# Performance work log

Hardware: AMD Instinct MI355X
Metric: run time of the kernel (lower is better)

Reference implementation:

```python
import jax, jax.numpy as jnp
import numpy as np

B, T, N, F_IN = 4, 8, 2048, 16
HID, HEADS, OUT_CH, OUT_FEAT = 128, 4, 64, 14
E = 32768


def _ln(x, g, b, eps=1e-5):
    mu = x.mean(-1, keepdims=True)
    var = ((x - mu) ** 2).mean(-1, keepdims=True)
    return (x - mu) / jnp.sqrt(var + eps) * g + b


def _attn_steps(x, wq, bq, wk, bk, wv, bv, wo, bo):
    # x: [B, S, M, F]; single-head causal attention over axis 1 (the 'steps' axis)
    q = x @ wq + bq
    k = x @ wk + bk
    v = x @ wv + bv
    scale = 1.0 / np.sqrt(q.shape[-1]).astype(np.float32)
    scores = jnp.einsum('bsmh,btmh->bmst', q, k) * scale  # [B,M,S,S]
    S = scores.shape[-1]
    scores = jnp.where(jnp.tril(jnp.ones((S, S), bool)), scores, -jnp.inf)
    a = jax.nn.softmax(scores, axis=-1)
    ctx = jnp.einsum('bmst,btmh->bsmh', a, v)
    return ctx @ wo + bo


def _attn_nodes(x, wq, bq, wk, bk, wv, bv, wo, bo):
    # single-head attention over axis 2 (the 'nodes' axis)
    q = x @ wq + bq
    k = x @ wk + bk
    v = x @ wv + bv
    scale = 1.0 / np.sqrt(q.shape[-1]).astype(np.float32)
    scores = jnp.einsum('bsnh,bsmh->bsnm', q, k) * scale
    a = jax.nn.softmax(scores, axis=-1)
    ctx = jnp.einsum('bsnm,bsmh->bsnh', a, v)
    return ctx @ wo + bo


def _gat(h, src, dst, n, W, a_src, a_dst, bias, heads, out_ch, concat):
    # PyG GATConv: gather src/dst features per edge, segment softmax over
    # incoming edges of each target node, weighted scatter-aggregate.
    hw = (h @ W).reshape(n, heads, out_ch)
    al_s = (hw * a_src).sum(-1)  # [n, heads]
    al_d = (hw * a_dst).sum(-1)
    loop = jnp.arange(n, dtype=src.dtype)
    src_f = jnp.concatenate([src, loop])
    dst_f = jnp.concatenate([dst, loop])
    alpha = jax.nn.leaky_relu(al_s[src_f] + al_d[dst_f], 0.2)
    # PyG removes pre-existing self-loops then adds canonical ones: mask them out.
    drop = jnp.concatenate([src == dst, jnp.zeros((n,), bool)])[:, None]
    amax = jax.lax.stop_gradient(
        jax.ops.segment_max(jnp.where(drop, -jnp.inf, alpha), dst_f, num_segments=n))
    ex = jnp.where(drop, 0.0, jnp.exp(alpha - amax[dst_f]))
    denom = jax.ops.segment_sum(ex, dst_f, num_segments=n)
    w = ex / denom[dst_f]  # [E_total, heads]
    out = jax.ops.segment_sum(hw[src_f] * w[:, :, None], dst_f, num_segments=n)
    if concat:
        return out.reshape(n, heads * out_ch) + bias
    return out.mean(1) + bias


def _forward(x, edge_index, ln1_g, ln1_b, t_wq, t_bq, t_wk, t_bk, t_wv, t_bv, t_wo, t_bo,
             skip_w, skip_b, ln2_g, ln2_b, s_wq, s_bq, s_wk, s_bk, s_wv, s_bv, s_wo, s_bo,
             ln3_g, ln3_b, mlp_w1, mlp_b1, mlp_w2, mlp_b2,
             gat1_w, gat1_asrc, gat1_adst, gat1_b, gat2_w, gat2_asrc, gat2_adst, gat2_b,
             ffn_w, ffn_b):
    Bx, Tx, Nx, _ = x.shape
    h = jnp.transpose(x, (0, 2, 1, 3))  # [B, N(steps), T(nodes), F]
    h = (h @ skip_w + skip_b) + _attn_steps(_ln(h, ln1_g, ln1_b),
                                            t_wq, t_bq, t_wk, t_bk, t_wv, t_bv, t_wo, t_bo)
    h = h + _attn_nodes(_ln(h, ln2_g, ln2_b), s_wq, s_bq, s_wk, s_bk, s_wv, s_bv, s_wo, s_bo)
    z = _ln(h, ln3_g, ln3_b)
    h = h + (jax.nn.relu(z @ mlp_w1 + mlp_b1) @ mlp_w2 + mlp_b2)
    h = h[:, :, -1, :].reshape(Bx * Nx, HID)  # last 'nodes'(=T) slot, flatten graphs
    src, dst = edge_index[0], edge_index[1]
    off = jnp.repeat(jnp.arange(Bx, dtype=src.dtype) * Nx, src.shape[0])
    src_b = jnp.tile(src, Bx) + off
    dst_b = jnp.tile(dst, Bx) + off
    nt = Bx * Nx
    g1 = jax.nn.elu(_gat(h, src_b, dst_b, nt, gat1_w, gat1_asrc, gat1_adst, gat1_b,
                         HEADS, HID // HEADS, True))
    g2 = _gat(g1, src_b, dst_b, nt, gat2_w, gat2_asrc, gat2_adst, gat2_b, 1, OUT_CH, False)
    out = g2.reshape(Bx, Nx, OUT_CH) @ ffn_w + ffn_b
    return jnp.transpose(out, (0, 2, 1))  # [B, output_features, N]


def setup_inputs():
    key = jax.random.key(0)
    ki = iter(list(jax.random.split(key, 40)))
    def rn(shape, s=0.05):
        return jax.random.normal(next(ki), shape, jnp.float32) * s
    d = {}
    d['x'] = jax.random.normal(next(ki), (B, T, N, F_IN), jnp.float32)
    d['edge_index'] = jax.random.randint(next(ki), (2, E), 0, N, jnp.int32)
    d['ln1_g'] = jnp.ones((F_IN,), jnp.float32); d['ln1_b'] = jnp.zeros((F_IN,), jnp.float32)
    d['t_wq'] = rn((F_IN, HID)); d['t_bq'] = jnp.zeros((HID,), jnp.float32)
    d['t_wk'] = rn((F_IN, HID)); d['t_bk'] = jnp.zeros((HID,), jnp.float32)
    d['t_wv'] = rn((F_IN, HID)); d['t_bv'] = jnp.zeros((HID,), jnp.float32)
    d['t_wo'] = rn((HID, HID)); d['t_bo'] = jnp.zeros((HID,), jnp.float32)
    d['skip_w'] = rn((F_IN, HID)); d['skip_b'] = jnp.zeros((HID,), jnp.float32)
    d['ln2_g'] = jnp.ones((HID,), jnp.float32); d['ln2_b'] = jnp.zeros((HID,), jnp.float32)
    d['s_wq'] = rn((HID, HID)); d['s_bq'] = jnp.zeros((HID,), jnp.float32)
    d['s_wk'] = rn((HID, HID)); d['s_bk'] = jnp.zeros((HID,), jnp.float32)
    d['s_wv'] = rn((HID, HID)); d['s_bv'] = jnp.zeros((HID,), jnp.float32)
    d['s_wo'] = rn((HID, HID)); d['s_bo'] = jnp.zeros((HID,), jnp.float32)
    d['ln3_g'] = jnp.ones((HID,), jnp.float32); d['ln3_b'] = jnp.zeros((HID,), jnp.float32)
    d['mlp_w1'] = rn((HID, 2 * HID)); d['mlp_b1'] = jnp.zeros((2 * HID,), jnp.float32)
    d['mlp_w2'] = rn((2 * HID, HID)); d['mlp_b2'] = jnp.zeros((HID,), jnp.float32)
    d['gat1_w'] = rn((HID, HID))
    d['gat1_asrc'] = rn((HEADS, HID // HEADS)); d['gat1_adst'] = rn((HEADS, HID // HEADS))
    d['gat1_b'] = jnp.zeros((HID,), jnp.float32)
    d['gat2_w'] = rn((HID, OUT_CH))
    d['gat2_asrc'] = rn((1, OUT_CH)); d['gat2_adst'] = rn((1, OUT_CH))
    d['gat2_b'] = jnp.zeros((OUT_CH,), jnp.float32)
    d['ffn_w'] = rn((OUT_CH, OUT_FEAT)); d['ffn_b'] = jnp.zeros((OUT_FEAT,), jnp.float32)
    return d


def reference(x, edge_index, ln1_g, ln1_b, t_wq, t_bq, t_wk, t_bk, t_wv, t_bv, t_wo, t_bo,
              skip_w, skip_b, ln2_g, ln2_b, s_wq, s_bq, s_wk, s_bk, s_wv, s_bv, s_wo, s_bo,
              ln3_g, ln3_b, mlp_w1, mlp_b1, mlp_w2, mlp_b2,
              gat1_w, gat1_asrc, gat1_adst, gat1_b, gat2_w, gat2_asrc, gat2_adst, gat2_b,
              ffn_w, ffn_b):
    return _forward(x, edge_index, ln1_g, ln1_b, t_wq, t_bq, t_wk, t_bk, t_wv, t_bv, t_wo, t_bo,
                    skip_w, skip_b, ln2_g, ln2_b, s_wq, s_bq, s_wk, s_bk, s_wv, s_bv, s_wo, s_bo,
                    ln3_g, ln3_b, mlp_w1, mlp_b1, mlp_w2, mlp_b2,
                    gat1_w, gat1_asrc, gat1_adst, gat1_b, gat2_w, gat2_asrc, gat2_adst, gat2_b,
                    ffn_w, ffn_b)
```

## Files before the change

kernel.cpp:

```cpp
#include <hip/hip_runtime.h>
#include <hip/hip_bf16.h>
#include <stdint.h>


#define BB     4
#define TT     8
#define NN     2048
#define FIN    16
#define HID    128
#define BM     (BB*TT)
#define PROWS  (BM*NN)
#define NHEADS 4
#define OUTCH  64
#define OUTF   14
#define NEDGE  32768
#define NEDGEB (NEDGE*BB)
#define NNODE  (BB*NN)
#define NETOT  (NEDGEB + NNODE)

#define TQ     64
#define NTILE  (NN/TQ)

typedef __hip_bfloat16 bf16;
typedef __attribute__((ext_vector_type(8))) short bf16x8;
typedef __attribute__((ext_vector_type(4))) float f32x4;

__device__ __forceinline__ float b2f(bf16 v){ return __bfloat162float(v); }
__device__ __forceinline__ bf16  f2b(float f){ return __float2bfloat16(f); }
__device__ __forceinline__ unsigned short bfbits(float f){
    union { bf16 h; unsigned short u; } cv; cv.h = f2b(f); return cv.u;
}

__global__ __launch_bounds__(256)
void k_kv(const float* __restrict__ x,
          const float* __restrict__ g1, const float* __restrict__ bb1,
          const float* __restrict__ wk, const float* __restrict__ bk,
          const float* __restrict__ wv, const float* __restrict__ bv,
          int in_off, bf16* __restrict__ K, bf16* __restrict__ Vt)
{
    const int r0 = blockIdx.x * 32;
    const int t  = threadIdx.x;

    __shared__ float wk_s[FIN][HID];
    __shared__ float wv_s[FIN][HID];
    __shared__ float xr_s[32][FIN+1];
    __shared__ float ln_s[32][FIN+1];

    #pragma unroll
    for (int it = 0; it < 2; ++it){
        const int u = t + it*256;
        ((float4*)wk_s)[u] = ((const float4*)wk)[u];
        ((float4*)wv_s)[u] = ((const float4*)wv)[u];
    }
    #pragma unroll
    for (int it = 0; it < 2; ++it){
        const int u = t + it*256;
        xr_s[u >> 4][u & 15] = x[(size_t)(r0 + in_off)*FIN + u];
    }
    __syncthreads();

    if (t < 32){
        float mu = 0.f;
        #pragma unroll
        for (int f = 0; f < FIN; ++f) mu += xr_s[t][f];
        mu *= (1.f/FIN);
        float var = 0.f;
        #pragma unroll
        for (int f = 0; f < FIN; ++f){ float d = xr_s[t][f]-mu; var += d*d; }
        var *= (1.f/FIN);
        const float inv = rsqrtf(var + 1e-5f);
        #pragma unroll
        for (int f = 0; f < FIN; ++f)
            ln_s[t][f] = (xr_s[t][f]-mu)*inv*g1[f] + bb1[f];
    }
    __syncthreads();

    {
        const int hk = (t & 63)*2;
        const float2 bkv = *(const float2*)&bk[hk];
        #pragma unroll
        for (int pass = 0; pass < 8; ++pass){
            const int key = pass*4 + (t >> 6);
            float a0 = bkv.x, a1 = bkv.y;
            #pragma unroll
            for (int f = 0; f < FIN; ++f){
                const float l = ln_s[key][f];
                const float2 wkv = ((const float2*)&wk_s[f][0])[t & 63];
                a0 += l*wkv.x; a1 += l*wkv.y;
            }
            const unsigned int pk =
                (unsigned int)bfbits(a0) | ((unsigned int)bfbits(a1) << 16);
            *(unsigned int*)(void*)&K[((size_t)(r0 + key))*HID + hk] = pk;
        }
    }

    {
        const int slice = r0 >> 11;
        const int kg    = (r0 & (NN-1)) >> 5;
        const size_t vbase = ((size_t)slice*(NN/32) + kg)*(size_t)HID*32;
        const int kk = (t & 15)*2;
        #pragma unroll
        for (int pass = 0; pass < 8; ++pass){
            const int h = (t >> 4) + 16*pass;
            float a0 = bv[h], a1 = a0;
            #pragma unroll
            for (int f = 0; f < FIN; ++f){
                const float wvf = wv_s[f][h];
                a0 += ln_s[kk  ][f] * wvf;
                a1 += ln_s[kk+1][f] * wvf;
            }
            const unsigned int pk =
                (unsigned int)bfbits(a0) | ((unsigned int)bfbits(a1) << 16);
            *(unsigned int*)(void*)&Vt[vbase + (size_t)h*32 + kk] = pk;
        }
    }
}

__global__ __launch_bounds__(256)
void k_attn_mfma(const float* __restrict__ x,
                 const bf16* __restrict__ K, const bf16* __restrict__ Vt,
                 const float* __restrict__ g1, const float* __restrict__ bb1,
                 const float* __restrict__ wq, const float* __restrict__ bq,
                 int slice_off, bf16* __restrict__ CX)
{
    const int tile  = (NTILE-1) - (int)blockIdx.y;
    const int q0    = tile*TQ;
    const int slice = blockIdx.x + slice_off;
    const int t     = threadIdx.x;
    const int w     = t >> 6;
    const int lane  = t & 63;
    const int quad  = lane >> 4;
    const int l16   = lane & 15;
    const int wr0   = w*16;

    const float qscale = 0.08838834764831845f * 1.4426950408889634f;

    __shared__ float xs [TQ][FIN+1];
    __shared__ bf16  Qs [TQ][136];
    __shared__ bf16  Ps [4][16][40];
    __shared__ __align__(16) bf16 KVs[32*136 + 128*40];
    bf16* Ks = KVs;
    bf16* Vs = KVs + 32*136;
    bf16 (*wqs)[32] = (bf16(*)[32])(&KVs[0]);
    bf16 (*xsb)[32] = (bf16(*)[32])(&KVs[4096]);

    const size_t kb = (size_t)blockIdx.x * NN * HID;
    const size_t vb = (size_t)blockIdx.x * (size_t)(NN/32) * HID*32;
    const bf16* kptr = K  + kb + (size_t)t*8;
    const bf16* vptr = Vt + vb + (size_t)t*8;
    bf16x8 kreg0, kreg1, vreg0, vreg1;
    kreg0 = *(const bf16x8*)(const void*)(kptr);
    kreg1 = *(const bf16x8*)(const void*)(kptr + 2048);
    vreg0 = *(const bf16x8*)(const void*)(vptr);
    vreg1 = *(const bf16x8*)(const void*)(vptr + 2048);

    #pragma unroll
    for (int it = 0; it < 4; ++it){
        const int u = t + it*256;
        xs[u >> 4][u & 15] = x[((size_t)slice*NN + q0)*FIN + u];
    }
    #pragma unroll
    for (int it = 0; it < 8; ++it){
        const int u = t + it*256;
        const int f = u >> 7, ch = u & 127;
        wqs[ch][f] = f2b(wq[u] * qscale);
    }
    {
        const bf16x8 z8 = {0,0,0,0,0,0,0,0};
        const int ch = t >> 1, k0 = 16 + (t & 1)*8;
        *(bf16x8*)(void*)&wqs[ch][k0] = z8;
    }
    __syncthreads();

    if (t < TQ){
        float mu = 0.f;
        #pragma unroll
        for (int f = 0; f < FIN; ++f) mu += xs[t][f];
        mu *= (1.f/FIN);
        float var = 0.f;
        #pragma unroll
        for (int f = 0; f < FIN; ++f){ float d = xs[t][f]-mu; var += d*d; }
        var *= (1.f/FIN);
        const float inv = rsqrtf(var + 1e-5f);
        bf16x8 v0, v1;
        #pragma unroll
        for (int f = 0; f < 8; ++f)
            v0[f] = (short)bfbits((xs[t][f]-mu)*inv*g1[f] + bb1[f]);
        #pragma unroll
        for (int f = 0; f < 8; ++f)
            v1[f] = (short)bfbits((xs[t][8+f]-mu)*inv*g1[8+f] + bb1[8+f]);
        const bf16x8 z8 = {0,0,0,0,0,0,0,0};
        *(bf16x8*)(void*)&xsb[t][0]  = v0;
        *(bf16x8*)(void*)&xsb[t][8]  = v1;
        *(bf16x8*)(void*)&xsb[t][16] = z8;
        *(bf16x8*)(void*)&xsb[t][24] = z8;
    }
    __syncthreads();

    {
        const bf16x8 af = *(const bf16x8*)(const void*)&xsb[wr0 + l16][quad*8];
        f32x4 Cq[8];
        #pragma unroll
        for (int ct = 0; ct < 8; ++ct){
            const bf16x8 bfv = *(const bf16x8*)(const void*)&wqs[ct*16 + l16][quad*8];
            Cq[ct] = __builtin_amdgcn_mfma_f32_16x16x32_bf16(
                         af, bfv, (f32x4){0.f,0.f,0.f,0.f}, 0, 0, 0);
        }
        #pragma unroll
        for (int ct = 0; ct < 8; ++ct){
            const int col = ct*16 + l16;
            const float bqs = bq[col] * qscale;
            #pragma unroll
            for (int r = 0; r < 4; ++r)
                Qs[wr0 + quad*4 + r][col] = f2b(Cq[ct][r] + bqs);
        }
    }
    __syncthreads();

    bf16x8 qf[4];
    #pragma unroll
    for (int ks = 0; ks < 4; ++ks)
        qf[ks] = *(const bf16x8*)(const void*)&Qs[wr0 + l16][ks*32 + quad*8];

    f32x4 O[8];
    #pragma unroll
    for (int ct = 0; ct < 8; ++ct) O[ct] = (f32x4){0.f,0.f,0.f,0.f};
    float l_[4] = {0.f,0.f,0.f,0.f};

    const int jend_blk = q0 + TQ - 1;
    const int my_jmax  = q0 + wr0 + 15;
    const int brow = q0 + wr0 + quad*4;

    bf16* ksA = &Ks[((t      ) >> 4)*136 + ((t      ) & 15)*8];
    bf16* ksB = &Ks[((t + 256) >> 4)*136 + ((t + 256) & 15)*8];
    bf16* vsA = &Vs[((t      ) >> 2)*40  + ((t      ) &  3)*8];
    bf16* vsB = &Vs[((t + 256) >> 2)*40  + ((t + 256) &  3)*8];
    const bf16* kr0 = &Ks[(2*l16    )*136 + quad*8];
    const bf16* kr1 = &Ks[(2*l16 + 1)*136 + quad*8];
    const bf16* vr  = &Vs[l16*40 + quad*8];

    for (int j0 = 0; j0 <= jend_blk; j0 += 32){
        *(bf16x8*)(void*)ksA = kreg0;
        *(bf16x8*)(void*)ksB = kreg1;
        *(bf16x8*)(void*)vsA = vreg0;
        *(bf16x8*)(void*)vsB = vreg1;
        __syncthreads();

        if (j0 + 32 <= jend_blk){
            const size_t off = (size_t)(j0 + 32)*128;
            kreg0 = *(const bf16x8*)(const void*)(kptr + off);
            kreg1 = *(const bf16x8*)(const void*)(kptr + off + 2048);
            vreg0 = *(const bf16x8*)(const void*)(vptr + off);
            vreg1 = *(const bf16x8*)(const void*)(vptr + off + 2048);
        }

        if (j0 <= my_jmax){
            f32x4 S0 = (f32x4){0.f,0.f,0.f,0.f}, S1 = S0;
            #pragma unroll
            for (int ks = 0; ks < 4; ++ks){
                const bf16x8 kf0 = *(const bf16x8*)(const void*)(kr0 + ks*32);
                const bf16x8 kf1 = *(const bf16x8*)(const void*)(kr1 + ks*32);
                S0 = __builtin_amdgcn_mfma_f32_16x16x32_bf16(qf[ks], kf0, S0, 0, 0, 0);
                S1 = __builtin_amdgcn_mfma_f32_16x16x32_bf16(qf[ks], kf1, S1, 0, 0, 0);
            }
            float sv0[4], sv1[4];
            if (j0 + 31 > q0 + wr0){
                const int c0j = j0 + 2*l16, c1j = c0j + 1;
                #pragma unroll
                for (int r = 0; r < 4; ++r){
                    sv0[r] = (c0j <= brow + r) ? S0[r] : -1e30f;
                    sv1[r] = (c1j <= brow + r) ? S1[r] : -1e30f;
                }
            } else {
                #pragma unroll
                for (int r = 0; r < 4; ++r){ sv0[r] = S0[r]; sv1[r] = S1[r]; }
            }
            #pragma unroll
            for (int r = 0; r < 4; ++r){
                const float e0 = __builtin_amdgcn_exp2f(sv0[r]);
                const float e1 = __builtin_amdgcn_exp2f(sv1[r]);
                l_[r] += e0 + e1;
                const unsigned int pk =
                    (unsigned int)bfbits(e0) | ((unsigned int)bfbits(e1) << 16);
                *(unsigned int*)(void*)&Ps[w][quad*4 + r][2*l16] = pk;
            }
            const bf16x8 pf = *(const bf16x8*)(const void*)&Ps[w][l16][quad*8];
            #pragma unroll
            for (int ct = 0; ct < 8; ++ct){
                const bf16x8 vf = *(const bf16x8*)(const void*)(vr + ct*16*40);
                O[ct] = __builtin_amdgcn_mfma_f32_16x16x32_bf16(pf, vf, O[ct], 0, 0, 0);
            }
        }
        __syncthreads();
    }

    {
        float inv[4];
        #pragma unroll
        for (int r = 0; r < 4; ++r){
            float rs = l_[r];
            rs += __shfl_xor(rs, 1);
            rs += __shfl_xor(rs, 2);
            rs += __shfl_xor(rs, 4);
            rs += __shfl_xor(rs, 8);
            inv[r] = 1.f/rs;
        }
        #pragma unroll
        for (int ct = 0; ct < 8; ++ct)
        #pragma unroll
        for (int r = 0; r < 4; ++r)
            Qs[wr0 + quad*4 + r][ct*16 + l16] = f2b(O[ct][r]*inv[r]);
    }
    __syncthreads();
    {
        const int row = t >> 2, ch0 = (t & 3)*32;
        bf16* dst = CX + ((size_t)slice*NN + q0 + row)*HID + ch0;
        #pragma unroll
        for (int c = 0; c < 4; ++c)
            *(bf16x8*)(void*)(dst + c*8) =
                *(const bf16x8*)(const void*)&Qs[row][ch0 + c*8];
    }
}

__global__ __launch_bounds__(256)
void k_h1(const float* __restrict__ x,
          const float* __restrict__ t_wo, const float* __restrict__ skw,
          const float* __restrict__ t_bo, const float* __restrict__ skb,
          int slice_off, bf16* __restrict__ CXH1)
{
    const int slice = blockIdx.x + slice_off;
    const int q0    = blockIdx.y * TQ;
    const int t     = threadIdx.x;
    const int w     = t >> 6;
    const int lane  = t & 63;
    const int quad  = lane >> 4;
    const int l16   = lane & 15;
    const int wr0   = w*16;

    __shared__ bf16 Aext[TQ][168];
    __shared__ bf16 Bext[HID][168];

    {
        const bf16* src = CXH1 + ((size_t)slice*NN + q0)*HID;
        #pragma unroll
        for (int it = 0; it < 4; ++it){
            const int c = t + it*256;
            *(bf16x8*)(void*)&Aext[c>>4][(c&15)*8] =
                *(const bf16x8*)(const void*)(src + c*8);
        }
    }
    #pragma unroll
    for (int it = 0; it < 4; ++it){
        const int u = t + it*256;
        const int row = u >> 4, f = u & 15;
        Aext[row][128 + f] = f2b(x[((size_t)slice*NN + q0 + row)*FIN + f]);
    }
    #pragma unroll
    for (int it = 0; it < 4; ++it){
        const int u = t + it*256;
        Aext[u>>4][144 + (u&15)] = f2b(0.f);
    }
    #pragma unroll
    for (int it = 0; it < 16; ++it){
        const int idx = t + it*256;
        const int c = idx >> 5, ch4 = (idx & 31)*4;
        const float4 v = ((const float4*)t_wo)[idx];
        Bext[ch4+0][c] = f2b(v.x);
        Bext[ch4+1][c] = f2b(v.y);
        Bext[ch4+2][c] = f2b(v.z);
        Bext[ch4+3][c] = f2b(v.w);
    }
    #pragma unroll
    for (int it = 0; it < 2; ++it){
        const int idx = t + it*256;
        const int f = idx >> 5, ch4 = (idx & 31)*4;
        const float4 v = ((const float4*)skw)[idx];
        Bext[ch4+0][128+f] = f2b(v.x);
        Bext[ch4+1][128+f] = f2b(v.y);
        Bext[ch4+2][128+f] = f2b(v.z);
        Bext[ch4+3][128+f] = f2b(v.w);
    }
    #pragma unroll
    for (int it = 0; it < 8; ++it){
        const int u = t + it*256;
        Bext[u>>4][144 + (u&15)] = f2b(0.f);
    }
    __syncthreads();

    f32x4 O[8];
    #pragma unroll
    for (int ct = 0; ct < 8; ++ct) O[ct] = (f32x4){0.f,0.f,0.f,0.f};
    #pragma unroll
    for (int ks = 0; ks < 5; ++ks){
        const bf16x8 af = *(const bf16x8*)(const void*)&Aext[wr0 + l16][ks*32 + quad*8];
        #pragma unroll
        for (int ct = 0; ct < 8; ++ct){
            const bf16x8 bf = *(const bf16x8*)(const void*)&Bext[ct*16 + l16][ks*32 + quad*8];
            O[ct] = __builtin_amdgcn_mfma_f32_16x16x32_bf16(af, bf, O[ct], 0, 0, 0);
        }
    }
    #pragma unroll
    for (int ct = 0; ct < 8; ++ct){
        const int col = ct*16 + l16;
        const float bias = t_bo[col] + skb[col];
        #pragma unroll
        for (int r = 0; r < 4; ++r)
            Aext[wr0 + quad*4 + r][col] = f2b(O[ct][r] + bias);
    }
    __syncthreads();
    {
        const int row = t >> 2, ch0 = (t & 3)*32;
        bf16* dst = CXH1 + ((size_t)slice*NN + q0 + row)*HID + ch0;
        #pragma unroll
        for (int c = 0; c < 4; ++c)
            *(bf16x8*)(void*)(dst + c*8) =
                *(const bf16x8*)(const void*)&Aext[row][ch0 + c*8];
    }
}

__global__ __launch_bounds__(256)
void k_prep(const float* __restrict__ s_wq, const float* __restrict__ s_wk,
            const float* __restrict__ bq, const float* __restrict__ bk,
            const float* __restrict__ s_wv, const float* __restrict__ s_wo,
            const float* __restrict__ g1w, const float* __restrict__ w1,
            const float* __restrict__ w2,
            bf16* __restrict__ Mt, bf16* __restrict__ wvT, bf16* __restrict__ woT,
            bf16* __restrict__ g1wT, bf16* __restrict__ w1T, bf16* __restrict__ w2T,
            float* __restrict__ vk, float* __restrict__ vq, float* __restrict__ sbb,
            float* __restrict__ zp, int zn)
{
    const int b = blockIdx.x;
    const int t = threadIdx.x;
    for (int u = b*256 + t; u < zn; u += 32*256) zp[u] = 0.f;
    __shared__ float wq_s[HID*HID];
    __shared__ float wk_s[8][HID];
    if (b < 16){
        for (int u = t; u < HID*HID; u += 256) wq_s[u] = s_wq[u];
        for (int u = t; u < 8*HID;   u += 256) ((float*)wk_s)[u] = s_wk[b*8*HID + u];
        __syncthreads();
        #pragma unroll
        for (int i = 0; i < 4; ++i){
            const int e = t + i*256;
            const int cl = e >> 7, a = e & 127;
            float acc = 0.f;
            for (int hh = 0; hh < HID; ++hh) acc += wk_s[cl][hh]*wq_s[a*HID + hh];
            Mt[(size_t)(b*8 + cl)*HID + a] = f2b(acc);
        }
    } else if (b == 16){
        if (t < HID){
            float a1 = 0.f, a2 = 0.f;
            for (int hh = 0; hh < HID; ++hh){
                a1 += bq[hh]*s_wk[t*HID + hh];
                a2 += s_wq[t*HID + hh]*bk[hh];
            }
            vk[t] = a1; vq[t] = a2;
            if (t == 0){
                float s = 0.f;
                for (int hh = 0; hh < HID; ++hh) s += bq[hh]*bk[hh];
                *sbb = s;
            }
        }
    } else if (b == 17){
        for (int u = t; u < HID*HID; u += 256){
            const int c = u >> 7, h = u & 127;
            wvT[h*HID + c] = f2b(s_wv[u]);
        }
    } else if (b == 18){
        for (int u = t; u < HID*HID; u += 256){
            const int c = u >> 7, h = u & 127;
            woT[h*HID + c] = f2b(s_wo[u]);
        }
    } else if (b == 19){
        for (int u = t; u < HID*HID; u += 256){
            const int c = u >> 7, h = u & 127;
            g1wT[h*HID + c] = f2b(g1w[u]);
        }
    } else if (b == 20){
        for (int u = t; u < HID*2*HID; u += 256){
            const int k = u >> 8, n = u & 255;
            w1T[n*HID + k] = f2b(w1[u]);
        }
    } else if (b == 21){
        for (int u = t; u < 2*HID*HID; u += 256){
            const int k = u >> 7, n = u & 127;
            w2T[(size_t)n*2*HID + k] = f2b(w2[u]);
        }
    }
}

__global__ __launch_bounds__(256)
void k_mix(const bf16* __restrict__ H1,
           const float* __restrict__ ln2g, const float* __restrict__ ln2b,
           const bf16* __restrict__ Mt, const bf16* __restrict__ wvT,
           const bf16* __restrict__ woT, const bf16* __restrict__ g1wT,
           const bf16* __restrict__ w1T, const bf16* __restrict__ w2T,
           const float* __restrict__ vk, const float* __restrict__ vq,
           const float* __restrict__ sbbp,
           const float* __restrict__ s_bv, const float* __restrict__ s_bo,
           const float* __restrict__ bm1, const float* __restrict__ bm2,
           const float* __restrict__ ln3g, const float* __restrict__ ln3b,
           const float* __restrict__ g1as, const float* __restrict__ g1ad,
           bf16* __restrict__ hw1, float* __restrict__ als1, float* __restrict__ ald1)
{
    const int blk0 = blockIdx.x * 16;
    const int bb = blk0 >> 11, s0 = blk0 & (NN-1);
    const int t = threadIdx.x;
    const int w = t >> 6;
    const int lane = t & 63;
    const int quad = lane >> 4;
    const int l16  = lane & 15;

    __shared__ bf16  h1s[16][TT][136];
    __shared__ bf16  ZA [16][136];
    __shared__ bf16  HLs[16][264];
    __shared__ float Cw [16][128];
    __shared__ float ln2gs[HID], ln2bs[HID];
    __shared__ float mu_s[16][TT], inv_s[16][TT];
    __shared__ float ps[16][TT];
    __shared__ float sbq_s[16], mu3[16], inv3[16];

    for (int m = 0; m < TT; ++m){
        const bf16* src = H1 + ((size_t)(bb*TT + m)*NN + s0)*HID;
        const int node = t >> 4, c8 = t & 15;
        *(bf16x8*)(void*)&h1s[node][m][c8*8] =
            *(const bf16x8*)(const void*)(src + (size_t)node*HID + c8*8);
    }
    if (t < HID){ ln2gs[t] = ln2g[t]; ln2bs[t] = ln2b[t]; }
    __syncthreads();

    {
        const int idx = t >> 1, half = t & 1;
        const int node = idx >> 3, m = idx & 7;
        float sum = 0.f, sq = 0.f;
        for (int c = half; c < HID; c += 2){
            const float v = b2f(h1s[node][m][c]);
            sum += v; sq += v*v;
        }
        sum += __shfl_xor(sum, 1); sq += __shfl_xor(sq, 1);
        if (half == 0){
            const float mu = sum*(1.f/HID);
            const float var = sq*(1.f/HID) - mu*mu;
            mu_s[node][m] = mu;
            inv_s[node][m] = rsqrtf(var + 1e-5f);
        }
    }
    __syncthreads();

    #pragma unroll
    for (int i = 0; i < 8; ++i){
        const int idx = t + i*256;
        const int n = idx >> 7, c = idx & 127;
        const float z = (b2f(h1s[n][7][c]) - mu_s[n][7])*inv_s[n][7]*ln2gs[c] + ln2bs[c];
        ZA[n][c] = f2b(z);
    }
    if (t < 128){
        const int node = t >> 3, l8 = t & 7;
        float sp = 0.f;
        for (int c = l8; c < HID; c += 8){
            const float z = (b2f(h1s[node][7][c]) - mu_s[node][7])*inv_s[node][7]*ln2gs[c] + ln2bs[c];
            sp += vq[c]*z;
        }
        sp += __shfl_xor(sp, 1);
        sp += __shfl_xor(sp, 2);
        sp += __shfl_xor(sp, 4);
        if (l8 == 0) sbq_s[node] = sp;
    }
    __syncthreads();

    {
        bf16x8 af[4];
        #pragma unroll
        for (int ks = 0; ks < 4; ++ks)
            af[ks] = *(const bf16x8*)(const void*)&ZA[l16][ks*32 + quad*8];
        __syncthreads();
        f32x4 C0 = (f32x4){0,0,0,0}, C1 = C0;
        #pragma unroll
        for (int ks = 0; ks < 4; ++ks){
            const bf16x8 b0 = *(const bf16x8*)(const void*)(Mt + (size_t)(w*32      + l16)*HID + ks*32 + quad*8);
            const bf16x8 b1 = *(const bf16x8*)(const void*)(Mt + (size_t)(w*32 + 16 + l16)*HID + ks*32 + quad*8);
            C0 = __builtin_amdgcn_mfma_f32_16x16x32_bf16(af[ks], b0, C0, 0, 0, 0);
            C1 = __builtin_amdgcn_mfma_f32_16x16x32_bf16(af[ks], b1, C1, 0, 0, 0);
        }
        const int c0 = w*32 + l16, c1 = c0 + 16;
        #pragma unroll
        for (int r = 0; r < 4; ++r){
            Cw[quad*4 + r][c0] = C0[r] + vk[c0];
            Cw[quad*4 + r][c1] = C1[r] + vk[c1];
        }
    }
    __syncthreads();

    {
        const int idx = t >> 1, half = t & 1;
        const int node = idx >> 3, m = idx & 7;
        const float mu = mu_s[node][m], iv = inv_s[node][m];
        float d = 0.f;
        for (int c = half; c < HID; c += 2){
            const float z = (b2f(h1s[node][m][c]) - mu)*iv*ln2gs[c] + ln2bs[c];
            d += Cw[node][c]*z;
        }
        d += __shfl_xor(d, 1);
        if (half == 0)
            ps[node][m] = (d + sbq_s[node] + *sbbp) * 0.08838834764831845f;
    }
    __syncthreads();
    if (t < 16){
        float mx = -1e30f;
        #pragma unroll
        for (int m = 0; m < TT; ++m) mx = fmaxf(mx, ps[t][m]);
        float p[TT], se = 0.f;
        #pragma unroll
        for (int m = 0; m < TT; ++m){ p[m] = __expf(ps[t][m]-mx); se += p[m]; }
        const float isum = 1.f/se;
        #pragma unroll
        for (int m = 0; m < TT; ++m) ps[t][m] = p[m]*isum;
    }
    __syncthreads();
    #pragma unroll
    for (int i = 0; i < 8; ++i){
        const int idx = t + i*256;
        const int n = idx >> 7, c = idx & 127;
        const float gc = ln2gs[c], bc = ln2bs[c];
        float acc = 0.f;
        #pragma unroll
        for (int m = 0; m < TT; ++m){
            const float z = (b2f(h1s[n][m][c]) - mu_s[n][m])*inv_s[n][m]*gc + bc;
            acc += ps[n][m]*z;
        }
        ZA[n][c] = f2b(acc);
    }
    __syncthreads();

    {
        bf16x8 af[4];
        #pragma unroll
        for (int ks = 0; ks < 4; ++ks)
            af[ks] = *(const bf16x8*)(const void*)&ZA[l16][ks*32 + quad*8];
        __syncthreads();
        f32x4 C0 = (f32x4){0,0,0,0}, C1 = C0;
        #pragma unroll
        for (int ks = 0; ks < 4; ++ks){
            const bf16x8 b0 = *(const bf16x8*)(const void*)(wvT + (size_t)(w*32      + l16)*HID + ks*32 + quad*8);
            const bf16x8 b1 = *(const bf16x8*)(const void*)(wvT + (size_t)(w*32 + 16 + l16)*HID + ks*32 + quad*8);
            C0 = __builtin_amdgcn_mfma_f32_16x16x32_bf16(af[ks], b0, C0, 0, 0, 0);
            C1 = __builtin_amdgcn_mfma_f32_16x16x32_bf16(af[ks], b1, C1, 0, 0, 0);
        }
        const int c0 = w*32 + l16, c1 = c0 + 16;
        #pragma unroll
        for (int r = 0; r < 4; ++r){
            ZA[quad*4 + r][c0] = f2b(C0[r] + s_bv[c0]);
            ZA[quad*4 + r][c1] = f2b(C1[r] + s_bv[c1]);
        }
    }
    __syncthreads();

    {
        bf16x8 af[4];
        #pragma unroll
        for (int ks = 0; ks < 4; ++ks)
            af[ks] = *(const bf16x8*)(const void*)&ZA[l16][ks*32 + quad*8];
        __syncthreads();
        f32x4 C0 = (f32x4){0,0,0,0}, C1 = C0;
        #pragma unroll
        for (int ks = 0; ks < 4; ++ks){
            const bf16x8 b0 = *(const bf16x8*)(const void*)(woT + (size_t)(w*32      + l16)*HID + ks*32 + quad*8);
            const bf16x8 b1 = *(const bf16x8*)(const void*)(woT + (size_t)(w*32 + 16 + l16)*HID + ks*32 + quad*8);
            C0 = __builtin_amdgcn_mfma_f32_16x16x32_bf16(af[ks], b0, C0, 0, 0, 0);
            C1 = __builtin_amdgcn_mfma_f32_16x16x32_bf16(af[ks], b1, C1, 0, 0, 0);
        }
        const int c0 = w*32 + l16, c1 = c0 + 16;
        #pragma unroll
        for (int r = 0; r < 4; ++r){
            const int node = quad*4 + r;
            Cw[node][c0] = C0[r] + s_bo[c0] + b2f(h1s[node][7][c0]);
            Cw[node][c1] = C1[r] + s_bo[c1] + b2f(h1s[node][7][c1]);
        }
    }
    __syncthreads();

    {
        const int node = t >> 4, part = t & 15;
        float sum = 0.f, sq = 0.f;
        for (int c = part; c < HID; c += 16){
            const float v = Cw[node][c];
            sum += v; sq += v*v;
        }
        sum += __shfl_xor(sum, 1); sq += __shfl_xor(sq, 1);
        sum += __shfl_xor(sum, 2); sq += __shfl_xor(sq, 2);
        sum += __shfl_xor(sum, 4); sq += __shfl_xor(sq, 4);
        sum += __shfl_xor(sum, 8); sq += __shfl_xor(sq, 8);
        if (part == 0){
            const float mu = sum*(1.f/HID);
            const float var = sq*(1.f/HID) - mu*mu;
            mu3[node] = mu;
            inv3[node] = rsqrtf(var + 1e-5f);
        }
    }
    __syncthreads();
    #pragma unroll
    for (int i = 0; i < 8; ++i){
        const int idx = t + i*256;
        const int n = idx >> 7, c = idx & 127;
        ZA[n][c] = f2b((Cw[n][c] - mu3[n])*inv3[n]*ln3g[c] + ln3b[c]);
    }
    __syncthreads();

    {
        bf16x8 af[4];
        #pragma unroll
        for (int ks = 0; ks < 4; ++ks)
            af[ks] = *(const bf16x8*)(const void*)&ZA[l16][ks*32 + quad*8];
        __syncthreads();
        f32x4 C[4];
        #pragma unroll
        for (int u = 0; u < 4; ++u) C[u] = (f32x4){0,0,0,0};
        #pragma unroll
        for (int ks = 0; ks < 4; ++ks){
            #pragma unroll
            for (int u = 0; u < 4; ++u){
                const bf16x8 bfv = *(const bf16x8*)(const void*)
                    (w1T + (size_t)(w*64 + u*16 + l16)*HID + ks*32 + quad*8);
                C[u] = __builtin_amdgcn_mfma_f32_16x16x32_bf16(af[ks], bfv, C[u], 0, 0, 0);
            }
        }
        #pragma unroll
        for (int u = 0; u < 4; ++u){
            const int col = w*64 + u*16 + l16;
            const float bias = bm1[col];
            #pragma unroll
            for (int r = 0; r < 4; ++r)
                HLs[quad*4 + r][col] = f2b(fmaxf(C[u][r] + bias, 0.f));
        }
    }
    __syncthreads();

    {
        bf16x8 af[8];
        #pragma unroll
        for (int ks = 0; ks < 8; ++ks)
            af[ks] = *(const bf16x8*)(const void*)&HLs[l16][ks*32 + quad*8];
        __syncthreads();
        f32x4 C0 = (f32x4){0,0,0,0}, C1 = C0;
        #pragma unroll
        for (int ks = 0; ks < 8; ++ks){
            const bf16x8 b0 = *(const bf16x8*)(const void*)(w2T + (size_t)(w*32      + l16)*2*HID + ks*32 + quad*8);
            const bf16x8 b1 = *(const bf16x8*)(const void*)(w2T + (size_t)(w*32 + 16 + l16)*2*HID + ks*32 + quad*8);
            C0 = __builtin_amdgcn_mfma_f32_16x16x32_bf16(af[ks], b0, C0, 0, 0, 0);
            C1 = __builtin_amdgcn_mfma_f32_16x16x32_bf16(af[ks], b1, C1, 0, 0, 0);
        }
        const int c0 = w*32 + l16, c1 = c0 + 16;
        #pragma unroll
        for (int r = 0; r < 4; ++r){
            const int node = quad*4 + r;
            ZA[node][c0] = f2b(C0[r] + bm2[c0] + Cw[node][c0]);
            ZA[node][c1] = f2b(C1[r] + bm2[c1] + Cw[node][c1]);
        }
    }
    __syncthreads();

    {
        bf16x8 af[4];
        #pragma unroll
        for (int ks = 0; ks < 4; ++ks)
            af[ks] = *(const bf16x8*)(const void*)&ZA[l16][ks*32 + quad*8];
        __syncthreads();
        f32x4 C0 = (f32x4){0,0,0,0}, C1 = C0;
        #pragma unroll
        for (int ks = 0; ks < 4; ++ks){
            const bf16x8 b0 = *(const bf16x8*)(const void*)(g1wT + (size_t)(w*32      + l16)*HID + ks*32 + quad*8);
            const bf16x8 b1 = *(const bf16x8*)(const void*)(g1wT + (size_t)(w*32 + 16 + l16)*HID + ks*32 + quad*8);
            C0 = __builtin_amdgcn_mfma_f32_16x16x32_bf16(af[ks], b0, C0, 0, 0, 0);
            C1 = __builtin_amdgcn_mfma_f32_16x16x32_bf16(af[ks], b1, C1, 0, 0, 0);
        }
        const int c0 = w*32 + l16, c1 = c0 + 16;
        #pragma unroll
        for (int r = 0; r < 4; ++r){
            Cw[quad*4 + r][c0] = C0[r];
            Cw[quad*4 + r][c1] = C1[r];
        }
    }
    __syncthreads();

    #pragma unroll
    for (int i = 0; i < 8; ++i){
        const int idx = t + i*256;
        hw1[(size_t)blk0*HID + idx] = f2b(((const float*)Cw)[idx]);
    }
    if (t < 64){
        const int node = t >> 2, hd = t & 3;
        float s1 = 0.f, s2 = 0.f;
        for (int j = 0; j < 32; ++j){
            const int c = hd*32 + j;
            const float a = Cw[node][c];
            s1 += a*g1as[c];
            s2 += a*g1ad[c];
        }
        als1[(blk0 + node)*NHEADS + hd] = s1;
        ald1[(blk0 + node)*NHEADS + hd] = s2;
    }
}

__global__ void k_csr_hist(const int* __restrict__ ei, int* __restrict__ cnt)
{
    const int e = blockIdx.x*blockDim.x + threadIdx.x;
    if (e >= NEDGE) return;
    const int s = ei[e], d = ei[NEDGE + e];
    if (s != d) atomicAdd(&cnt[d], 1);
}

__global__ __launch_bounds__(256)
void k_csr_scan(const int* __restrict__ cnt, int* __restrict__ roff)
{
    const int t = threadIdx.x;
    __shared__ int part[256];
    int loc[8]; int s = 0;
    #pragma unroll
    for (int i = 0; i < 8; ++i){ loc[i] = s; s += cnt[t*8 + i]; }
    part[t] = s;
    __syncthreads();
    if (t == 0){
        int acc = 0;
        for (int i = 0; i < 256; ++i){ const int v = part[i]; part[i] = acc; acc += v; }
    }
    __syncthreads();
    const int base_ = part[t];
    #pragma unroll
    for (int i = 0; i < 8; ++i) roff[t*8 + i] = base_ + loc[i];
    if (t == 255) roff[2048] = base_ + s;
}

__global__ void k_csr_scatter(const int* __restrict__ ei, const int* __restrict__ roff,
                              int* __restrict__ fill, int* __restrict__ col)
{
    const int e = blockIdx.x*blockDim.x + threadIdx.x;
    if (e >= NEDGE) return;
    const int s = ei[e], d = ei[NEDGE + e];
    if (s != d){
        const int p = roff[d] + atomicAdd(&fill[d], 1);
        col[p] = s;
    }
}

__global__ __launch_bounds__(128)
void k_gat_gather1(const int* __restrict__ roff, const int* __restrict__ col,
                   const float* __restrict__ als, const float* __restrict__ ald,
                   const bf16* __restrict__ hw, const float* __restrict__ g1b,
                   float* __restrict__ hr)
{
    const int nid = blockIdx.x;
    const int d   = nid & (NN-1);
    const int gb  = nid & ~(NN-1);
    const int c   = threadIdx.x;
    const int hd  = c >> 5;
    const float ad = ald[nid*NHEADS + hd];

    float accv = 0.f, accd = 0.f;
    const int e0 = roff[d], e1 = roff[d+1];
    int sn = (e0 < e1) ? col[e0] : 0;
    for (int e = e0; e < e1; ++e){
        const int s = sn + gb;
        sn = (e+1 < e1) ? col[e+1] : 0;
        float a = als[s*NHEADS + hd] + ad;
        a = a > 0.f ? a : 0.2f*a;
        const float ex = __expf(a);
        accv += ex * b2f(hw[(size_t)s*HID + c]);
        accd += ex;
    }
    {
        float a = als[nid*NHEADS + hd] + ad;
        a = a > 0.f ? a : 0.2f*a;
        const float ex = __expf(a);
        accv += ex * b2f(hw[(size_t)nid*HID + c]);
        accd += ex;
    }
    const float v = accv/accd + g1b[c];
    hr[(size_t)nid*HID + c] = v > 0.f ? v : expm1f(v);
}

__global__ void k_gat2_lin(const float* __restrict__ hr,
                           const float* __restrict__ W,
                           const float* __restrict__ asrc, const float* __restrict__ adst,
                           bf16* __restrict__ hw2, float* __restrict__ al2s, float* __restrict__ al2d)
{
    const int nid = blockIdx.x, c = threadIdx.x;
    __shared__ float hrs[HID];
    hrs[c]      = hr[(size_t)nid*HID + c];
    hrs[c + 64] = hr[(size_t)nid*HID + c + 64];
    __syncthreads();
    float a = 0.f;
    for (int k = 0; k < HID; ++k) a += hrs[k]*W[k*OUTCH + c];
    hw2[(size_t)nid*OUTCH + c] = f2b(a);
    float s1 = a*asrc[c], s2 = a*adst[c];
    #pragma unroll
    for (int off = 32; off > 0; off >>= 1){
        s1 += __shfl_down(s1, off);
        s2 += __shfl_down(s2, off);
    }
    if (c == 0){ al2s[nid] = s1; al2d[nid] = s2; }
}

__global__ __launch_bounds__(64)
void k_gat_gather2f(const int* __restrict__ roff, const int* __restrict__ col,
                    const float* __restrict__ als, const float* __restrict__ ald,
                    const bf16* __restrict__ hw2, const float* __restrict__ g2b,
                    const float* __restrict__ fw, const float* __restrict__ fb,
                    float* __restrict__ out)
{
    const int nid = blockIdx.x;
    const int d   = nid & (NN-1);
    const int gb  = nid & ~(NN-1);
    const int c   = threadIdx.x;
    const float ad = ald[nid];

    float accv = 0.f, accd = 0.f;
    const int e0 = roff[d], e1 = roff[d+1];
    int sn = (e0 < e1) ? col[e0] : 0;
    for (int e = e0; e < e1; ++e){
        const int s = sn + gb;
        sn = (e+1 < e1) ? col[e+1] : 0;
        float a = als[s] + ad;
        a = a > 0.f ? a : 0.2f*a;
        const float ex = __expf(a);
        accv += ex * b2f(hw2[(size_t)s*OUTCH + c]);
        accd += ex;
    }
    {
        float a = als[nid] + ad;
        a = a > 0.f ? a : 0.2f*a;
        const float ex = __expf(a);
        accv += ex * b2f(hw2[(size_t)nid*OUTCH + c]);
        accd += ex;
    }
    __shared__ float g[OUTCH];
    g[c] = accv/accd + g2b[c];
    __syncthreads();
    if (c < OUTF){
        float o = fb[c];
        #pragma unroll
        for (int k = 0; k < OUTCH; ++k) o += g[k]*fw[k*OUTF + c];
        const int b = nid >> 11, n = nid & (NN-1);
        out[((size_t)b*OUTF + c)*NN + n] = o;
    }
}

extern "C" void kernel_launch(void* const* d_in, const int* in_sizes, int n_in,
                              void* d_out, int out_size, void* d_ws, size_t ws_size,
                              hipStream_t stream)
{
    const float* x    = (const float*)d_in[0];
    const int*  ei    = (const int*)d_in[1];
    const float* ln1g = (const float*)d_in[2];  const float* ln1b = (const float*)d_in[3];
    const float* t_wq = (const float*)d_in[4];  const float* t_bq = (const float*)d_in[5];
    const float* t_wk = (const float*)d_in[6];  const float* t_bk = (const float*)d_in[7];
    const float* t_wv = (const float*)d_in[8];  const float* t_bv = (const float*)d_in[9];
    const float* t_wo = (const float*)d_in[10]; const float* t_bo = (const float*)d_in[11];
    const float* skw  = (const float*)d_in[12]; const float* skb  = (const float*)d_in[13];
    const float* ln2g = (const float*)d_in[14]; const float* ln2b = (const float*)d_in[15];
    const float* s_wq = (const float*)d_in[16]; const float* s_bq = (const float*)d_in[17];
    const float* s_wk = (const float*)d_in[18]; const float* s_bk = (const float*)d_in[19];
    const float* s_wv = (const float*)d_in[20]; const float* s_bv = (const float*)d_in[21];
    const float* s_wo = (const float*)d_in[22]; const float* s_bo = (const float*)d_in[23];
    const float* ln3g = (const float*)d_in[24]; const float* ln3b = (const float*)d_in[25];
    const float* w1   = (const float*)d_in[26]; const float* b1   = (const float*)d_in[27];
    const float* w2   = (const float*)d_in[28]; const float* b2   = (const float*)d_in[29];
    const float* g1w  = (const float*)d_in[30];
    const float* g1as = (const float*)d_in[31]; const float* g1ad = (const float*)d_in[32];
    const float* g1b  = (const float*)d_in[33];
    const float* g2w  = (const float*)d_in[34];
    const float* g2as = (const float*)d_in[35]; const float* g2ad = (const float*)d_in[36];
    const float* g2b  = (const float*)d_in[37];
    const float* ffw  = (const float*)d_in[38]; const float* ffb  = (const float*)d_in[39];
    float* out = (float*)d_out;

    const size_t MiB = 1024u*1024u;
    const bool wide = ws_size >= 48*MiB;

    char* base = (char*)d_ws;
    bf16 *Kb, *Vtb, *CXH1;
    char* gat_base;
    char* mbase;
    if (wide){
        Kb   = (bf16*)(base + 0*MiB);
        Vtb  = (bf16*)(base + 16*MiB);
        CXH1 = (bf16*)(base + 32*MiB);
        gat_base = base;
        mbase = base + 13*MiB;
    } else {
        CXH1 = (bf16*)(base + 0*MiB);
        gat_base = base + 16*MiB;
        Kb   = (bf16*)(base + 26*MiB);
        Vtb  = (bf16*)(base + 26*MiB + 512u*1024u);
        mbase = base + 27*MiB;
    }
    bf16*  Mt   = (bf16*)mbase;
    bf16*  wvT  = (bf16*)(mbase + 32*1024);
    bf16*  woT  = (bf16*)(mbase + 64*1024);
    bf16*  g1wT = (bf16*)(mbase + 96*1024);
    bf16*  w1T  = (bf16*)(mbase + 128*1024);
    bf16*  w2T  = (bf16*)(mbase + 192*1024);
    float* vkw  = (float*)(mbase + 256*1024);
    float* vqw  = (float*)(mbase + 256*1024 + 512);
    float* sbb  = (float*)(mbase + 256*1024 + 1024);

    char* w = gat_base;
    auto alloc = [&](size_t bytes){ void* p = (void*)w; w += (bytes + 255) & ~(size_t)255; return p; };
    int*   cnt  = (int*)  alloc(2048u*sizeof(int));
    int*   fill = (int*)  alloc(2048u*sizeof(int));
    char*  zend = w;
    int*   roff = (int*)  alloc(2049u*sizeof(int));
    int*   col  = (int*)  alloc((size_t)NEDGE*sizeof(int));
    float* hr   = (float*)alloc((size_t)NNODE*HID*sizeof(float));
    bf16*  hw1  = (bf16*) alloc((size_t)NNODE*HID*sizeof(bf16));
    float* als1 = (float*)alloc((size_t)NNODE*NHEADS*sizeof(float));
    float* ald1 = (float*)alloc((size_t)NNODE*NHEADS*sizeof(float));
    bf16*  hw2  = (bf16*) alloc((size_t)NNODE*OUTCH*sizeof(bf16));
    float* als2 = (float*)alloc((size_t)NNODE*sizeof(float));
    float* ald2 = (float*)alloc((size_t)NNODE*sizeof(float));
    const int zero_n = (int)((zend - (char*)cnt)/4);

    if (wide){
        k_kv<<<PROWS/32, 256, 0, stream>>>(x, ln1g, ln1b, t_wk, t_bk, t_wv, t_bv, 0, Kb, Vtb);
        k_attn_mfma<<<dim3(BM, NTILE), 256, 0, stream>>>(x, Kb, Vtb, ln1g, ln1b,
                                                         t_wq, t_bq, 0, CXH1);
        k_h1<<<dim3(BM, NTILE), 256, 0, stream>>>(x, t_wo, skw, t_bo, skb, 0, CXH1);
    } else {
        for (int s = 0; s < BM; ++s){
            k_kv<<<NN/32, 256, 0, stream>>>(x, ln1g, ln1b, t_wk, t_bk, t_wv, t_bv, s*NN, Kb, Vtb);
            k_attn_mfma<<<dim3(1, NTILE), 256, 0, stream>>>(x, Kb, Vtb, ln1g, ln1b,
                                                            t_wq, t_bq, s, CXH1);
        }
        k_h1<<<dim3(BM, NTILE), 256, 0, stream>>>(x, t_wo, skw, t_bo, skb, 0, CXH1);
    }
    k_prep<<<32, 256, 0, stream>>>(s_wq, s_wk, s_bq, s_bk, s_wv, s_wo, g1w, w1, w2,
                                   Mt, wvT, woT, g1wT, w1T, w2T,
                                   vkw, vqw, sbb, (float*)cnt, zero_n);

    k_csr_hist   <<<NEDGE/256, 256, 0, stream>>>(ei, cnt);
    k_csr_scan   <<<1,        256, 0, stream>>>(cnt, roff);
    k_csr_scatter<<<NEDGE/256, 256, 0, stream>>>(ei, roff, fill, col);

    k_mix<<<NNODE/16, 256, 0, stream>>>(CXH1, ln2g, ln2b, Mt, wvT, woT, g1wT, w1T, w2T,
                                        vkw, vqw, sbb, s_bv, s_bo, b1, b2,
                                        ln3g, ln3b, g1as, g1ad, hw1, als1, ald1);

    k_gat_gather1<<<NNODE, 128, 0, stream>>>(roff, col, als1, ald1, hw1, g1b, hr);
    k_gat2_lin   <<<NNODE,  64, 0, stream>>>(hr, g2w, g2as, g2ad, hw2, als2, ald2);
    k_gat_gather2f<<<NNODE, 64, 0, stream>>>(roff, col, als2, ald2, hw2, g2b, ffw, ffb, out);
}
```

Baseline: 409.1 us.

## Alias attention Q buffer into KV smem, precompute h1 weights, batch gat2_lin nodes

The attention kernel drops its separate Q shared buffer and reuses the K/V staging area, adding barriers so the writes do not race, which lowers LDS use and can raise occupancy. The k_h1 kernel stops transposing and converting t_wo/skw in every block. It reads a bf16 matrix prepared once by k_prep, which now runs before k_h1, directly from global memory. k_gat2_lin handles four nodes per 256-thread block instead of one node per 64-thread block. In exchange, k_h1 fetches its B operands from global or cache rather than LDS, and the extra syncs in attention add some serialization.

```diff
diff --git a/kernel.cpp b/kernel.cpp
--- a/kernel.cpp
+++ b/kernel.cpp
@@ -136,13 +136,13 @@
     const float qscale = 0.08838834764831845f * 1.4426950408889634f;
 
     __shared__ float xs [TQ][FIN+1];
-    __shared__ bf16  Qs [TQ][136];
     __shared__ bf16  Ps [4][16][40];
     __shared__ __align__(16) bf16 KVs[32*136 + 128*40];
     bf16* Ks = KVs;
     bf16* Vs = KVs + 32*136;
     bf16 (*wqs)[32] = (bf16(*)[32])(&KVs[0]);
     bf16 (*xsb)[32] = (bf16(*)[32])(&KVs[4096]);
+    bf16 (*Qv)[136] = (bf16(*)[136])(&KVs[0]);
 
     const size_t kb = (size_t)blockIdx.x * NN * HID;
     const size_t vb = (size_t)blockIdx.x * (size_t)(NN/32) * HID*32;
@@ -206,13 +206,14 @@
             Cq[ct] = __builtin_amdgcn_mfma_f32_16x16x32_bf16(
                          af, bfv, (f32x4){0.f,0.f,0.f,0.f}, 0, 0, 0);
         }
+        __syncthreads();
         #pragma unroll
         for (int ct = 0; ct < 8; ++ct){
             const int col = ct*16 + l16;
             const float bqs = bq[col] * qscale;
             #pragma unroll
             for (int r = 0; r < 4; ++r)
-                Qs[wr0 + quad*4 + r][col] = f2b(Cq[ct][r] + bqs);
+                Qv[wr0 + quad*4 + r][col] = f2b(Cq[ct][r] + bqs);
         }
     }
     __syncthreads();
@@ -220,7 +221,8 @@
     bf16x8 qf[4];
     #pragma unroll
     for (int ks = 0; ks < 4; ++ks)
-        qf[ks] = *(const bf16x8*)(const void*)&Qs[wr0 + l16][ks*32 + quad*8];
+        qf[ks] = *(const bf16x8*)(const void*)&Qv[wr0 + l16][ks*32 + quad*8];
+    __syncthreads();
 
     f32x4 O[8];
     #pragma unroll
@@ -309,7 +311,7 @@
         for (int ct = 0; ct < 8; ++ct)
         #pragma unroll
         for (int r = 0; r < 4; ++r)
-            Qs[wr0 + quad*4 + r][ct*16 + l16] = f2b(O[ct][r]*inv[r]);
+            Qv[wr0 + quad*4 + r][ct*16 + l16] = f2b(O[ct][r]*inv[r]);
     }
     __syncthreads();
     {
@@ -318,13 +320,13 @@
         #pragma unroll
         for (int c = 0; c < 4; ++c)
             *(bf16x8*)(void*)(dst + c*8) =
-                *(const bf16x8*)(const void*)&Qs[row][ch0 + c*8];
+                *(const bf16x8*)(const void*)&Qv[row][ch0 + c*8];
     }
 }
 
 __global__ __launch_bounds__(256)
 void k_h1(const float* __restrict__ x,
-          const float* __restrict__ t_wo, const float* __restrict__ skw,
+          const bf16* __restrict__ BH1,
           const float* __restrict__ t_bo, const float* __restrict__ skb,
           int slice_off, bf16* __restrict__ CXH1)
 {
@@ -338,7 +340,6 @@
     const int wr0   = w*16;
 
     __shared__ bf16 Aext[TQ][168];
-    __shared__ bf16 Bext[HID][168];
 
     {
         const bf16* src = CXH1 + ((size_t)slice*NN + q0)*HID;
@@ -360,31 +361,6 @@
         const int u = t + it*256;
         Aext[u>>4][144 + (u&15)] = f2b(0.f);
     }
-    #pragma unroll
-    for (int it = 0; it < 16; ++it){
-        const int idx = t + it*256;
-        const int c = idx >> 5, ch4 = (idx & 31)*4;
-        const float4 v = ((const float4*)t_wo)[idx];
-        Bext[ch4+0][c] = f2b(v.x);
-        Bext[ch4+1][c] = f2b(v.y);
-        Bext[ch4+2][c] = f2b(v.z);
-        Bext[ch4+3][c] = f2b(v.w);
-    }
-    #pragma unroll
-    for (int it = 0; it < 2; ++it){
-        const int idx = t + it*256;
-        const int f = idx >> 5, ch4 = (idx & 31)*4;
-        const float4 v = ((const float4*)skw)[idx];
-        Bext[ch4+0][128+f] = f2b(v.x);
-        Bext[ch4+1][128+f] = f2b(v.y);
-        Bext[ch4+2][128+f] = f2b(v.z);
-        Bext[ch4+3][128+f] = f2b(v.w);
-    }
-    #pragma unroll
-    for (int it = 0; it < 8; ++it){
-        const int u = t + it*256;
-        Bext[u>>4][144 + (u&15)] = f2b(0.f);
-    }
     __syncthreads();
 
     f32x4 O[8];
@@ -395,10 +371,12 @@
         const bf16x8 af = *(const bf16x8*)(const void*)&Aext[wr0 + l16][ks*32 + quad*8];
         #pragma unroll
         for (int ct = 0; ct < 8; ++ct){
-            const bf16x8 bf = *(const bf16x8*)(const void*)&Bext[ct*16 + l16][ks*32 + quad*8];
+            const bf16x8 bf = *(const bf16x8*)(const void*)
+                (BH1 + (size_t)(ct*16 + l16)*168 + ks*32 + quad*8);
             O[ct] = __builtin_amdgcn_mfma_f32_16x16x32_bf16(af, bf, O[ct], 0, 0, 0);
         }
     }
+    __syncthreads();
     #pragma unroll
     for (int ct = 0; ct < 8; ++ct){
         const int col = ct*16 + l16;
@@ -424,8 +402,10 @@
             const float* __restrict__ s_wv, const float* __restrict__ s_wo,
             const float* __restrict__ g1w, const float* __restrict__ w1,
             const float* __restrict__ w2,
+            const float* __restrict__ t_wo, const float* __restrict__ skw,
             bf16* __restrict__ Mt, bf16* __restrict__ wvT, bf16* __restrict__ woT,
             bf16* __restrict__ g1wT, bf16* __restrict__ w1T, bf16* __restrict__ w2T,
+            bf16* __restrict__ BH1,
             float* __restrict__ vk, float* __restrict__ vq, float* __restrict__ sbb,
             float* __restrict__ zp, int zn)
 {
@@ -485,6 +465,14 @@
             const int k = u >> 7, n = u & 127;
             w2T[(size_t)n*2*HID + k] = f2b(w2[u]);
         }
+    } else if (b == 22){
+        for (int u = t; u < HID*168; u += 256){
+            const int c = u / 168, k = u - c*168;
+            float v = 0.f;
+            if (k < 128)      v = t_wo[k*HID + c];
+            else if (k < 144) v = skw[(k-128)*HID + c];
+            BH1[u] = f2b(v);
+        }
     }
 }
 
@@ -877,18 +865,20 @@
     hr[(size_t)nid*HID + c] = v > 0.f ? v : expm1f(v);
 }
 
-__global__ void k_gat2_lin(const float* __restrict__ hr,
-                           const float* __restrict__ W,
-                           const float* __restrict__ asrc, const float* __restrict__ adst,
-                           bf16* __restrict__ hw2, float* __restrict__ al2s, float* __restrict__ al2d)
-{
-    const int nid = blockIdx.x, c = threadIdx.x;
-    __shared__ float hrs[HID];
-    hrs[c]      = hr[(size_t)nid*HID + c];
-    hrs[c + 64] = hr[(size_t)nid*HID + c + 64];
-    __syncthreads();
+__global__ __launch_bounds__(256)
+void k_gat2_lin(const float* __restrict__ hr,
+                const float* __restrict__ W,
+                const float* __restrict__ asrc, const float* __restrict__ adst,
+                bf16* __restrict__ hw2, float* __restrict__ al2s, float* __restrict__ al2d)
+{
+    const int wv  = threadIdx.x >> 6;
+    const int c   = threadIdx.x & 63;
+    const int nid = blockIdx.x*4 + wv;
+    __shared__ float hrs[4][HID];
+    hrs[wv][c]      = hr[(size_t)nid*HID + c];
+    hrs[wv][c + 64] = hr[(size_t)nid*HID + c + 64];
     float a = 0.f;
-    for (int k = 0; k < HID; ++k) a += hrs[k]*W[k*OUTCH + c];
+    for (int k = 0; k < HID; ++k) a += hrs[wv][k]*W[k*OUTCH + c];
     hw2[(size_t)nid*OUTCH + c] = f2b(a);
     float s1 = a*asrc[c], s2 = a*adst[c];
     #pragma unroll
@@ -1001,6 +991,7 @@
     float* vkw  = (float*)(mbase + 256*1024);
     float* vqw  = (float*)(mbase + 256*1024 + 512);
     float* sbb  = (float*)(mbase + 256*1024 + 1024);
+    bf16*  BH1  = (bf16*)(mbase + 272*1024);
 
     char* w = gat_base;
     auto alloc = [&](size_t bytes){ void* p = (void*)w; w += (bytes + 255) & ~(size_t)255; return p; };
@@ -1022,18 +1013,23 @@
         k_kv<<<PROWS/32, 256, 0, stream>>>(x, ln1g, ln1b, t_wk, t_bk, t_wv, t_bv, 0, Kb, Vtb);
         k_attn_mfma<<<dim3(BM, NTILE), 256, 0, stream>>>(x, Kb, Vtb, ln1g, ln1b,
                                                          t_wq, t_bq, 0, CXH1);
-        k_h1<<<dim3(BM, NTILE), 256, 0, stream>>>(x, t_wo, skw, t_bo, skb, 0, CXH1);
+        k_prep<<<32, 256, 0, stream>>>(s_wq, s_wk, s_bq, s_bk, s_wv, s_wo, g1w, w1, w2,
+                                       t_wo, skw,
+                                       Mt, wvT, woT, g1wT, w1T, w2T, BH1,
+                                       vkw, vqw, sbb, (float*)cnt, zero_n);
+        k_h1<<<dim3(BM, NTILE), 256, 0, stream>>>(x, BH1, t_bo, skb, 0, CXH1);
     } else {
         for (int s = 0; s < BM; ++s){
             k_kv<<<NN/32, 256, 0, stream>>>(x, ln1g, ln1b, t_wk, t_bk, t_wv, t_bv, s*NN, Kb, Vtb);
             k_attn_mfma<<<dim3(1, NTILE), 256, 0, stream>>>(x, Kb, Vtb, ln1g, ln1b,
                                                             t_wq, t_bq, s, CXH1);
         }
-        k_h1<<<dim3(BM, NTILE), 256, 0, stream>>>(x, t_wo, skw, t_bo, skb, 0, CXH1);
-    }
-    k_prep<<<32, 256, 0, stream>>>(s_wq, s_wk, s_bq, s_bk, s_wv, s_wo, g1w, w1, w2,
-                                   Mt, wvT, woT, g1wT, w1T, w2T,
-                                   vkw, vqw, sbb, (float*)cnt, zero_n);
+        k_prep<<<32, 256, 0, stream>>>(s_wq, s_wk, s_bq, s_bk, s_wv, s_wo, g1w, w1, w2,
+                                       t_wo, skw,
+                                       Mt, wvT, woT, g1wT, w1T, w2T, BH1,
+                                       vkw, vqw, sbb, (float*)cnt, zero_n);
+        k_h1<<<dim3(BM, NTILE), 256, 0, stream>>>(x, BH1, t_bo, skb, 0, CXH1);
+    }
 
     k_csr_hist   <<<NEDGE/256, 256, 0, stream>>>(ei, cnt);
     k_csr_scan   <<<1,        256, 0, stream>>>(cnt, roff);
@@ -1044,6 +1040,6 @@
                                         ln3g, ln3b, g1as, g1ad, hw1, als1, ald1);
 
     k_gat_gather1<<<NNODE, 128, 0, stream>>>(roff, col, als1, ald1, hw1, g1b, hr);
-    k_gat2_lin   <<<NNODE,  64, 0, stream>>>(hr, g2w, g2as, g2ad, hw2, als2, ald2);
+    k_gat2_lin   <<<NNODE/4, 256, 0, stream>>>(hr, g2w, g2as, g2ad, hw2, als2, ald2);
     k_gat_gather2f<<<NNODE, 64, 0, stream>>>(roff, col, als2, ald2, hw2, g2b, ffw, ffb, out);
 }
```

Measured after the change: 405.9 us. About the same (-0.8%).
